# Optimization experiments

Measured on AMD Instinct MI355X. Metric: run time of the kernel, lower is better.

The kernel has to match this reference:

```python
import jax, jax.numpy as jnp
import numpy as np

H = 256
W = 256
RADIUS = 1.5
TAU = 1.0
EPS = 1e-8


def _ndc_grid(h, w):
    ys, xs = jnp.meshgrid(jnp.arange(h, dtype=jnp.float32), jnp.arange(w, dtype=jnp.float32), indexing='ij')
    xs = xs / (w - 1) * 2.0 - 1.0
    ys = ys / (h - 1) * 2.0 - 1.0
    return jnp.stack([xs.ravel(), ys.ravel()], 0)  # [2, N]


def _make_rt(key, b, v):
    # near-identity extrinsics: identity rotation + small random translation
    t = jax.random.normal(key, (b, v, 3), dtype=jnp.float32) * 0.05
    rt = jnp.tile(jnp.eye(4, dtype=jnp.float32), (b, v, 1, 1))
    rt = rt.at[:, :, :3, 3].set(t)
    return rt


def setup_inputs() -> dict:
    key = jax.random.key(0)
    ks = jax.random.split(key, 4)
    B, V, C = 2, 3, 32
    depths = jax.random.uniform(ks[0], (B, V, 1, H, W), jnp.float32, 1.0, 3.0)
    feats = jax.random.normal(ks[1], (B, V, C, H, W), jnp.float32)
    K = jnp.tile(jnp.eye(4, dtype=jnp.float32), (B, 1, 1))
    K = K.at[:, 0, 0].set(1.2).at[:, 1, 1].set(1.2)  # NDC-space focal lengths
    src_RTs = _make_rt(ks[2], B, V)
    src_RTinvs = jnp.linalg.inv(src_RTs)
    dst_RTs = _make_rt(ks[3], B, 1)
    dst_RTinvs = jnp.linalg.inv(dst_RTs)
    return {"depths": depths, "feats": feats, "K": K, "src_RTs": src_RTs,
            "src_RTinvs": src_RTinvs, "dst_RTs": dst_RTs, "dst_RTinvs": dst_RTinvs}


def _view_to_world(depth, K_inv, RTinv):
    # depth: [BV, 1, N] -> world homogeneous coords [BV, 4, N]
    grid = _ndc_grid(H, W)                                      # [2, N]
    xy = grid[None] * depth                                     # [BV, 2, N]
    pc = jnp.concatenate([xy, depth, jnp.ones_like(depth)], 1)  # [BV, 4, N]
    cam = jnp.einsum('bij,bjn->bin', K_inv, pc)
    return jnp.einsum('bij,bjn->bin', RTinv, cam)


def _world_to_view(wrld, K, RT):
    cam = jnp.einsum('bij,bjn->bin', RT, wrld)
    proj = jnp.einsum('bij,bjn->bin', K, cam)
    z = proj[:, 2:3]
    xy = proj[:, 0:2] / (z + EPS)
    xy = jnp.where(z <= 0.0, -10.0, xy)       # invalid points pushed off-screen
    return jnp.concatenate([xy, z], 1)        # [BV, 3, N]


def _splatter(pc, feats, radius):
    # pc: [BV, N, 3] (x_ndc, y_ndc, depth); feats: [BV, C, N]
    BV, N, _ = pc.shape
    C = feats.shape[1]
    x, y, z = pc[..., 0], pc[..., 1], pc[..., 2]
    px = (x + 1.0) * 0.5 * (W - 1)
    py = (y + 1.0) * 0.5 * (H - 1)
    offs = jnp.array([[dy, dx] for dy in (-1, 0, 1) for dx in (-1, 0, 1)], dtype=jnp.float32)
    ix = jnp.round(px)[..., None] + offs[:, 1]     # [BV, N, 9]
    iy = jnp.round(py)[..., None] + offs[:, 0]
    dist = jnp.sqrt((ix - px[..., None]) ** 2 + (iy - py[..., None]) ** 2 + EPS)
    w_r = jnp.maximum(0.0, 1.0 - dist / radius)    # radius-based falloff
    valid = (ix >= 0) & (ix < W) & (iy >= 0) & (iy < H) & (z[..., None] > 0)
    w_d = jnp.exp(-TAU * z)[..., None]             # depth-aware (soft z-buffer) weight
    w = w_r * w_d * valid.astype(w_r.dtype)        # [BV, N, 9]
    idx = iy.astype(jnp.int32).clip(0, H - 1) * W + ix.astype(jnp.int32).clip(0, W - 1)
    flat = (jnp.arange(BV, dtype=jnp.int32)[:, None, None] * (H * W) + idx).reshape(-1)
    w_sum = jax.ops.segment_sum(w.reshape(-1), flat, num_segments=BV * H * W)
    fw = (feats[:, :, :, None] * w[:, None, :, :]).transpose(0, 2, 3, 1).reshape(-1, C)
    f_sum = jax.ops.segment_sum(fw, flat, num_segments=BV * H * W)
    z_sum = jax.ops.segment_sum((z[..., None] * w).reshape(-1), flat, num_segments=BV * H * W)
    out_f = (f_sum / (w_sum[:, None] + EPS)).reshape(BV, H, W, C).transpose(0, 3, 1, 2)
    out_d = (z_sum / (w_sum + EPS)).reshape(BV, 1, H, W)
    return out_f, out_d


def reference(depths, feats, K, src_RTs, src_RTinvs, dst_RTs, dst_RTinvs):
    B, V, C = feats.shape[0], feats.shape[1], feats.shape[2]
    N = H * W
    d = depths.reshape(B * V, 1, N)
    f = feats.reshape(B * V, C, N)
    K_bv = jnp.repeat(K, V, axis=0)
    K_inv_bv = jnp.repeat(jnp.linalg.inv(K), V, axis=0)
    src_rtinv = src_RTinvs.reshape(B * V, 4, 4)
    dst_rt = jnp.repeat(dst_RTs[:, 0], V, axis=0)
    wrld = _view_to_world(d, K_inv_bv, src_rtinv)      # view -> world per source view
    sampler = _world_to_view(wrld, K_bv, dst_rt)       # world -> target view [BV,3,N]
    pc = sampler.transpose(0, 2, 1)                    # [BV, N, 3]
    prj_f, prj_d = _splatter(pc, f, RADIUS)
    return prj_f.reshape(B, V, C, H, W), prj_d.reshape(B, V, 1, H, W)
```

## Files before the change

### kernel.cpp

```cpp
#include <hip/hip_runtime.h>
#include <hip/hip_fp16.h>
#include <math.h>

#define H 256
#define W 256
#define HW (H * W)
#define B 2
#define V 3
#define BV (B * V)
#define C 32
#define RADIUS 1.5f
#define TAU 1.0f
#define EPS 1e-8f

#define NPIX (BV * HW)
#define NBLK (NPIX / 256)
#define CAP 16
#define OVF_CAP 65536

__device__ __forceinline__ int swizzle_block(int bid) {
    return (bid & 7) * (NBLK / 8) + (bid >> 3);
}

__global__ void setup_kernel(const float* __restrict__ Kmat,
                             const float* __restrict__ srcRTinv,
                             const float* __restrict__ dstRT,
                             float* __restrict__ Mbuf) {
    int bv = threadIdx.x;
    if (bv >= BV) return;
    int b = bv / V;

    float a[4][8];
    for (int i = 0; i < 4; i++)
        for (int j = 0; j < 4; j++) {
            a[i][j] = Kmat[b * 16 + i * 4 + j];
            a[i][4 + j] = (i == j) ? 1.0f : 0.0f;
        }
    for (int col = 0; col < 4; col++) {
        int piv = col;
        float best = fabsf(a[col][col]);
        for (int r = col + 1; r < 4; r++) {
            float v = fabsf(a[r][col]);
            if (v > best) { best = v; piv = r; }
        }
        if (piv != col) {
            for (int j = 0; j < 8; j++) {
                float t = a[col][j]; a[col][j] = a[piv][j]; a[piv][j] = t;
            }
        }
        float s = 1.0f / a[col][col];
        for (int j = 0; j < 8; j++) a[col][j] *= s;
        for (int r = 0; r < 4; r++) {
            if (r == col) continue;
            float m = a[r][col];
            for (int j = 0; j < 8; j++) a[r][j] -= m * a[col][j];
        }
    }
    float Kinv[16];
    for (int i = 0; i < 4; i++)
        for (int j = 0; j < 4; j++) Kinv[i * 4 + j] = a[i][4 + j];

    float T1[16];
    const float* S = srcRTinv + bv * 16;
    for (int i = 0; i < 4; i++)
        for (int j = 0; j < 4; j++) {
            float acc = 0.0f;
            for (int k = 0; k < 4; k++) acc += S[i * 4 + k] * Kinv[k * 4 + j];
            T1[i * 4 + j] = acc;
        }
    float T2[16];
    const float* D = dstRT + b * 16;
    for (int i = 0; i < 4; i++)
        for (int j = 0; j < 4; j++) {
            float acc = 0.0f;
            for (int k = 0; k < 4; k++) acc += D[i * 4 + k] * T1[k * 4 + j];
            T2[i * 4 + j] = acc;
        }
    const float* Kb = Kmat + b * 16;
    for (int i = 0; i < 4; i++)
        for (int j = 0; j < 4; j++) {
            float acc = 0.0f;
            for (int k = 0; k < 4; k++) acc += Kb[i * 4 + k] * T2[k * 4 + j];
            Mbuf[bv * 16 + i * 4 + j] = acc;
        }
}

template <typename F>
__device__ __forceinline__ void for_each_tap(float px, float py, float z, F&& fn) {
    if (!(z > 0.0f)) return;
    float rx = rintf(px), ry = rintf(py);
#pragma unroll
    for (int dy = -1; dy <= 1; dy++) {
#pragma unroll
        for (int dx = -1; dx <= 1; dx++) {
            float ix = rx + (float)dx, iy = ry + (float)dy;
            if (ix >= 0.0f && ix < (float)W && iy >= 0.0f && iy < (float)H) {
                float ddx = ix - px, ddy = iy - py;
                float d2 = ddx * ddx + ddy * ddy + EPS;
                if (d2 < RADIUS * RADIUS) {
                    int q = ((int)iy << 8) | (int)ix;
                    fn(q);
                }
            }
        }
    }
}

__global__ __launch_bounds__(256) void project_fill_kernel(
    const float* __restrict__ depths, const float* __restrict__ Mbuf,
    int* __restrict__ counts, unsigned short* __restrict__ bins16,
    int* __restrict__ ovf_cnt, int2* __restrict__ ovf) {
    int gid = swizzle_block(blockIdx.x) * 256 + threadIdx.x;
    int bv = gid >> 16;
    int n = gid & (HW - 1);
    int pxi = n & (W - 1);
    int pyi = n >> 8;

    float xn = (float)pxi * (2.0f / (W - 1)) - 1.0f;
    float yn = (float)pyi * (2.0f / (H - 1)) - 1.0f;
    float d = depths[gid];
    const float* M = Mbuf + bv * 16;
    float X = xn * d, Y = yn * d;
    float p0 = M[0] * X + M[1] * Y + M[2] * d + M[3];
    float p1 = M[4] * X + M[5] * Y + M[6] * d + M[7];
    float z  = M[8] * X + M[9] * Y + M[10] * d + M[11];

    bool zpos = z > 0.0f;
    float inv = 1.0f / (z + EPS);
    float xp = zpos ? p0 * inv : -10.0f;
    float yp = zpos ? p1 * inv : -10.0f;
    float px = (xp + 1.0f) * 0.5f * (float)(W - 1);
    float py = (yp + 1.0f) * 0.5f * (float)(H - 1);

    int base = bv << 16;
    for_each_tap(px, py, z, [&](int q) {
        int g = base | q;
        int slot = atomicAdd(&counts[g], 1);
        if (slot < CAP) {
            bins16[(size_t)g * CAP + slot] = (unsigned short)n;
        } else {
            int o = atomicAdd(ovf_cnt, 1);
            if (o < OVF_CAP) ovf[o] = make_int2(g, n);
        }
    });
}

__global__ __launch_bounds__(256) void transpose_kernel(
    const float* __restrict__ feats, __half* __restrict__ featsT) {
    __shared__ float sm[C][257];
    int blk = blockIdx.x;
    int bv = blk >> 8;
    int n0 = (blk & 255) << 8;
    int tid = threadIdx.x;
    const float* src = feats + (size_t)bv * C * HW + n0;
#pragma unroll
    for (int c = 0; c < C; c++) sm[c][tid] = src[(size_t)c * HW + tid];
    __syncthreads();
    __half* dst = featsT + ((size_t)bv * HW + n0) * C;
#pragma unroll
    for (int pass = 0; pass < 8; pass++) {
        int nl = pass * 32 + (tid >> 3);
        int c4 = (tid & 7) << 2;
        __half2 lo = __floats2half2_rn(sm[c4][nl], sm[c4 + 1][nl]);
        __half2 hi = __floats2half2_rn(sm[c4 + 2][nl], sm[c4 + 3][nl]);
        uint2 pk;
        pk.x = *(unsigned int*)&lo;
        pk.y = *(unsigned int*)&hi;
        *(uint2*)(dst + (size_t)nl * C + c4) = pk;
    }
}

__global__ __launch_bounds__(256) void gather_kernel(
    const float* __restrict__ depths, const float* __restrict__ Mbuf,
    const __half* __restrict__ featsT, const int* __restrict__ counts,
    const unsigned short* __restrict__ bins16,
    const int* __restrict__ ovf_cnt, const int2* __restrict__ ovf,
    float* __restrict__ out) {
    int gid = swizzle_block(blockIdx.x) * 256 + threadIdx.x;
    int bv = gid >> 16;
    int q = gid & (HW - 1);
    float qx = (float)(q & (W - 1));
    float qy = (float)(q >> 8);

    int cnt = counts[gid];
    int cap = min(cnt, CAP);

    const float* M = Mbuf + bv * 16;
    float m00 = M[0], m01 = M[1], m02 = M[2],  m03 = M[3];
    float m10 = M[4], m11 = M[5], m12 = M[6],  m13 = M[7];
    float m20 = M[8], m21 = M[9], m22 = M[10], m23 = M[11];

    const float* dep = depths + ((size_t)bv << 16);
    const __half* fb = featsT + ((size_t)bv << 16) * C;

    float wsum = 0.0f, zwsum = 0.0f;
    float facc[C];
#pragma unroll
    for (int c = 0; c < C; c++) facc[c] = 0.0f;

    auto accumulate = [&](int n) {
        float d = dep[n];
        float xn = (float)(n & (W - 1)) * (2.0f / (W - 1)) - 1.0f;
        float yn = (float)(n >> 8)      * (2.0f / (H - 1)) - 1.0f;
        float X = xn * d, Y = yn * d;
        float p0 = m00 * X + m01 * Y + m02 * d + m03;
        float p1 = m10 * X + m11 * Y + m12 * d + m13;
        float z  = m20 * X + m21 * Y + m22 * d + m23;
        float inv = 1.0f / (z + EPS);
        float px = (p0 * inv + 1.0f) * 0.5f * (float)(W - 1);
        float py = (p1 * inv + 1.0f) * 0.5f * (float)(H - 1);
        float ddx = qx - px, ddy = qy - py;
        float dist = sqrtf(ddx * ddx + ddy * ddy + EPS);
        float wr = fmaxf(0.0f, 1.0f - dist * (1.0f / RADIUS));
        float w = wr * expf(-TAU * z);
        wsum += w;
        zwsum += z * w;
        const uint4* fp = (const uint4*)(fb + (size_t)n * C);
#pragma unroll
        for (int g = 0; g < 4; g++) {
            uint4 v = fp[g];
            const __half2* h2 = (const __half2*)&v;
#pragma unroll
            for (int k = 0; k < 4; k++) {
                float2 f2 = __half22float2(h2[k]);
                facc[g * 8 + 2 * k]     = fmaf(w, f2.x, facc[g * 8 + 2 * k]);
                facc[g * 8 + 2 * k + 1] = fmaf(w, f2.y, facc[g * 8 + 2 * k + 1]);
            }
        }
    };

    const uint4* bp = (const uint4*)(bins16 + (size_t)gid * CAP);
    uint4 r0 = bp[0];
    uint4 r1 = bp[1];
    auto do2 = [&](unsigned int wv, int j0) {
        if (j0 < cap)     accumulate((int)(wv & 0xffffu));
        if (j0 + 1 < cap) accumulate((int)(wv >> 16));
    };
    do2(r0.x, 0);  do2(r0.y, 2);  do2(r0.z, 4);  do2(r0.w, 6);
    do2(r1.x, 8);  do2(r1.y, 10); do2(r1.z, 12); do2(r1.w, 14);

    if (cnt > CAP) {
        int oc = min(*ovf_cnt, OVF_CAP);
        for (int i = 0; i < oc; i++) {
            int2 e = ovf[i];
            if (e.x == gid) accumulate(e.y);
        }
    }

    float invw = 1.0f / (wsum + EPS);
    float* ob = out + (size_t)bv * C * HW + q;
#pragma unroll
    for (int c = 0; c < C; c++) ob[(size_t)c * HW] = facc[c] * invw;
    out[(size_t)BV * C * HW + gid] = zwsum * invw;
}

extern "C" void kernel_launch(void* const* d_in, const int* in_sizes, int n_in,
                              void* d_out, int out_size, void* d_ws, size_t ws_size,
                              hipStream_t stream) {
    const float* depths   = (const float*)d_in[0];
    const float* feats    = (const float*)d_in[1];
    const float* Kmat     = (const float*)d_in[2];
    const float* srcRTinv = (const float*)d_in[4];
    const float* dstRT    = (const float*)d_in[5];
    float* out = (float*)d_out;

    char* ws = (char*)d_ws;
    size_t off_bins = 0;
    size_t off_featsT = off_bins + (size_t)CAP * NPIX * 2;
    size_t off_counts = off_featsT + (size_t)NPIX * C * 2;
    size_t off_ovfcnt = off_counts + (size_t)NPIX * 4;
    size_t off_ovf = off_ovfcnt + 16;
    size_t off_M = off_ovf + (size_t)OVF_CAP * 8;
    size_t needed = off_M + (size_t)BV * 16 * 4;

    if (ws_size < needed) {
        hipMemsetAsync(d_out, 0, (size_t)out_size * 4, stream);
        return;
    }

    unsigned short* bins16 = (unsigned short*)(ws + off_bins);
    __half* featsT = (__half*)(ws + off_featsT);
    int* counts    = (int*)(ws + off_counts);
    int* ovf_cnt   = (int*)(ws + off_ovfcnt);
    int2* ovf      = (int2*)(ws + off_ovf);
    float* Mbuf    = (float*)(ws + off_M);

    hipMemsetAsync(counts, 0, (size_t)NPIX * 4 + 16, stream);
    setup_kernel<<<1, 64, 0, stream>>>(Kmat, srcRTinv, dstRT, Mbuf);
    project_fill_kernel<<<NBLK, 256, 0, stream>>>(depths, Mbuf, counts, bins16,
                                                  ovf_cnt, ovf);
    transpose_kernel<<<NBLK, 256, 0, stream>>>(feats, featsT);
    gather_kernel<<<NBLK, 256, 0, stream>>>(depths, Mbuf, featsT, counts,
                                            bins16, ovf_cnt, ovf, out);
}
```

Baseline: 210.0 us.

## Bin each projected point once by nearest cell; gather scans 3x3 neighborhood

The fill pass now does one atomic insert per source point into its nearest pixel cell, on a padded grid, instead of up to nine atomics into per-target bins. The cell entry stores the index together with the depth. The gather kernel scans the 3x3 neighbouring cells, recomputes the projection, and skips points whose radial weight is zero. This removes most scatter atomics and the separate depth reload. In exchange, gather now reads nine counters and more candidate entries per pixel, and the per-cell capacity is smaller, so more points may spill into the linearly scanned overflow list.

Measured after the change: 197.1 us. -6.2%, faster.

```diff
diff --git a/kernel.cpp b/kernel.cpp
--- a/kernel.cpp
+++ b/kernel.cpp
@@ -15,7 +15,11 @@
 
 #define NPIX (BV * HW)
 #define NBLK (NPIX / 256)
-#define CAP 16
+
+#define GW 258
+#define GH 258
+#define NCELL (BV * GH * GW)
+#define CCAP 8
 #define OVF_CAP 65536
 
 __device__ __forceinline__ int swizzle_block(int bid) {
@@ -85,31 +89,10 @@
         }
 }
 
-template <typename F>
-__device__ __forceinline__ void for_each_tap(float px, float py, float z, F&& fn) {
-    if (!(z > 0.0f)) return;
-    float rx = rintf(px), ry = rintf(py);
-#pragma unroll
-    for (int dy = -1; dy <= 1; dy++) {
-#pragma unroll
-        for (int dx = -1; dx <= 1; dx++) {
-            float ix = rx + (float)dx, iy = ry + (float)dy;
-            if (ix >= 0.0f && ix < (float)W && iy >= 0.0f && iy < (float)H) {
-                float ddx = ix - px, ddy = iy - py;
-                float d2 = ddx * ddx + ddy * ddy + EPS;
-                if (d2 < RADIUS * RADIUS) {
-                    int q = ((int)iy << 8) | (int)ix;
-                    fn(q);
-                }
-            }
-        }
-    }
-}
-
 __global__ __launch_bounds__(256) void project_fill_kernel(
     const float* __restrict__ depths, const float* __restrict__ Mbuf,
-    int* __restrict__ counts, unsigned short* __restrict__ bins16,
-    int* __restrict__ ovf_cnt, int2* __restrict__ ovf) {
+    int* __restrict__ counts, float2* __restrict__ cells,
+    int* __restrict__ ovf_cnt, int4* __restrict__ ovf) {
     int gid = swizzle_block(blockIdx.x) * 256 + threadIdx.x;
     int bv = gid >> 16;
     int n = gid & (HW - 1);
@@ -125,24 +108,24 @@
     float p1 = M[4] * X + M[5] * Y + M[6] * d + M[7];
     float z  = M[8] * X + M[9] * Y + M[10] * d + M[11];
 
-    bool zpos = z > 0.0f;
+    if (!(z > 0.0f)) return;
     float inv = 1.0f / (z + EPS);
-    float xp = zpos ? p0 * inv : -10.0f;
-    float yp = zpos ? p1 * inv : -10.0f;
-    float px = (xp + 1.0f) * 0.5f * (float)(W - 1);
-    float py = (yp + 1.0f) * 0.5f * (float)(H - 1);
-
-    int base = bv << 16;
-    for_each_tap(px, py, z, [&](int q) {
-        int g = base | q;
-        int slot = atomicAdd(&counts[g], 1);
-        if (slot < CAP) {
-            bins16[(size_t)g * CAP + slot] = (unsigned short)n;
-        } else {
-            int o = atomicAdd(ovf_cnt, 1);
-            if (o < OVF_CAP) ovf[o] = make_int2(g, n);
-        }
-    });
+    float px = (p0 * inv + 1.0f) * 0.5f * (float)(W - 1);
+    float py = (p1 * inv + 1.0f) * 0.5f * (float)(H - 1);
+    float rx = rintf(px), ry = rintf(py);
+    if (rx < -1.0f || rx > (float)W || ry < -1.0f || ry > (float)H) return;
+
+    int cell = bv * (GH * GW) + ((int)ry + 1) * GW + ((int)rx + 1);
+    int slot = atomicAdd(&counts[cell], 1);
+    if (slot < CCAP) {
+        float2 e;
+        e.x = __uint_as_float((unsigned int)n);
+        e.y = d;
+        cells[(size_t)cell * CCAP + slot] = e;
+    } else {
+        int o = atomicAdd(ovf_cnt, 1);
+        if (o < OVF_CAP) ovf[o] = make_int4(cell, n, __float_as_int(d), 0);
+    }
 }
 
 __global__ __launch_bounds__(256) void transpose_kernel(
@@ -171,10 +154,9 @@
 }
 
 __global__ __launch_bounds__(256) void gather_kernel(
-    const float* __restrict__ depths, const float* __restrict__ Mbuf,
-    const __half* __restrict__ featsT, const int* __restrict__ counts,
-    const unsigned short* __restrict__ bins16,
-    const int* __restrict__ ovf_cnt, const int2* __restrict__ ovf,
+    const float* __restrict__ Mbuf, const __half* __restrict__ featsT,
+    const int* __restrict__ counts, const float2* __restrict__ cells,
+    const int* __restrict__ ovf_cnt, const int4* __restrict__ ovf,
     float* __restrict__ out) {
     int gid = swizzle_block(blockIdx.x) * 256 + threadIdx.x;
     int bv = gid >> 16;
@@ -182,15 +164,11 @@
     float qx = (float)(q & (W - 1));
     float qy = (float)(q >> 8);
 
-    int cnt = counts[gid];
-    int cap = min(cnt, CAP);
-
     const float* M = Mbuf + bv * 16;
     float m00 = M[0], m01 = M[1], m02 = M[2],  m03 = M[3];
     float m10 = M[4], m11 = M[5], m12 = M[6],  m13 = M[7];
     float m20 = M[8], m21 = M[9], m22 = M[10], m23 = M[11];
 
-    const float* dep = depths + ((size_t)bv << 16);
     const __half* fb = featsT + ((size_t)bv << 16) * C;
 
     float wsum = 0.0f, zwsum = 0.0f;
@@ -198,8 +176,7 @@
 #pragma unroll
     for (int c = 0; c < C; c++) facc[c] = 0.0f;
 
-    auto accumulate = [&](int n) {
-        float d = dep[n];
+    auto accumulate = [&](int n, float d) {
         float xn = (float)(n & (W - 1)) * (2.0f / (W - 1)) - 1.0f;
         float yn = (float)(n >> 8)      * (2.0f / (H - 1)) - 1.0f;
         float X = xn * d, Y = yn * d;
@@ -212,38 +189,46 @@
         float ddx = qx - px, ddy = qy - py;
         float dist = sqrtf(ddx * ddx + ddy * ddy + EPS);
         float wr = fmaxf(0.0f, 1.0f - dist * (1.0f / RADIUS));
-        float w = wr * expf(-TAU * z);
-        wsum += w;
-        zwsum += z * w;
-        const uint4* fp = (const uint4*)(fb + (size_t)n * C);
-#pragma unroll
-        for (int g = 0; g < 4; g++) {
-            uint4 v = fp[g];
-            const __half2* h2 = (const __half2*)&v;
-#pragma unroll
-            for (int k = 0; k < 4; k++) {
-                float2 f2 = __half22float2(h2[k]);
-                facc[g * 8 + 2 * k]     = fmaf(w, f2.x, facc[g * 8 + 2 * k]);
-                facc[g * 8 + 2 * k + 1] = fmaf(w, f2.y, facc[g * 8 + 2 * k + 1]);
+        if (wr > 0.0f) {
+            float w = wr * expf(-TAU * z);
+            wsum += w;
+            zwsum += z * w;
+            const uint4* fp = (const uint4*)(fb + (size_t)n * C);
+#pragma unroll
+            for (int g = 0; g < 4; g++) {
+                uint4 v = fp[g];
+                const __half2* h2 = (const __half2*)&v;
+#pragma unroll
+                for (int k = 0; k < 4; k++) {
+                    float2 f2 = __half22float2(h2[k]);
+                    facc[g * 8 + 2 * k]     = fmaf(w, f2.x, facc[g * 8 + 2 * k]);
+                    facc[g * 8 + 2 * k + 1] = fmaf(w, f2.y, facc[g * 8 + 2 * k + 1]);
+                }
             }
         }
     };
 
-    const uint4* bp = (const uint4*)(bins16 + (size_t)gid * CAP);
-    uint4 r0 = bp[0];
-    uint4 r1 = bp[1];
-    auto do2 = [&](unsigned int wv, int j0) {
-        if (j0 < cap)     accumulate((int)(wv & 0xffffu));
-        if (j0 + 1 < cap) accumulate((int)(wv >> 16));
-    };
-    do2(r0.x, 0);  do2(r0.y, 2);  do2(r0.z, 4);  do2(r0.w, 6);
-    do2(r1.x, 8);  do2(r1.y, 10); do2(r1.z, 12); do2(r1.w, 14);
-
-    if (cnt > CAP) {
-        int oc = min(*ovf_cnt, OVF_CAP);
-        for (int i = 0; i < oc; i++) {
-            int2 e = ovf[i];
-            if (e.x == gid) accumulate(e.y);
+    int cbase = bv * (GH * GW);
+#pragma unroll
+    for (int dy = 0; dy < 3; dy++) {
+        int rowbase = cbase + (q / W + dy) * GW + (q & (W - 1));
+#pragma unroll
+        for (int dx = 0; dx < 3; dx++) {
+            int cell = rowbase + dx;
+            int cc = counts[cell];
+            int m = min(cc, CCAP);
+            const float2* e = cells + (size_t)cell * CCAP;
+            for (int j = 0; j < m; j++) {
+                float2 v = e[j];
+                accumulate((int)__float_as_uint(v.x), v.y);
+            }
+            if (cc > CCAP) {
+                int oc = min(*ovf_cnt, OVF_CAP);
+                for (int i = 0; i < oc; i++) {
+                    int4 t = ovf[i];
+                    if (t.x == cell) accumulate(t.y, __int_as_float(t.z));
+                }
+            }
         }
     }
 
@@ -265,12 +250,12 @@
     float* out = (float*)d_out;
 
     char* ws = (char*)d_ws;
-    size_t off_bins = 0;
-    size_t off_featsT = off_bins + (size_t)CAP * NPIX * 2;
+    size_t off_cells = 0;
+    size_t off_featsT = off_cells + (size_t)NCELL * CCAP * 8;
     size_t off_counts = off_featsT + (size_t)NPIX * C * 2;
-    size_t off_ovfcnt = off_counts + (size_t)NPIX * 4;
+    size_t off_ovfcnt = off_counts + (size_t)NCELL * 4;
     size_t off_ovf = off_ovfcnt + 16;
-    size_t off_M = off_ovf + (size_t)OVF_CAP * 8;
+    size_t off_M = off_ovf + (size_t)OVF_CAP * 16;
     size_t needed = off_M + (size_t)BV * 16 * 4;
 
     if (ws_size < needed) {
@@ -278,18 +263,18 @@
         return;
     }
 
-    unsigned short* bins16 = (unsigned short*)(ws + off_bins);
+    float2* cells  = (float2*)(ws + off_cells);
     __half* featsT = (__half*)(ws + off_featsT);
     int* counts    = (int*)(ws + off_counts);
     int* ovf_cnt   = (int*)(ws + off_ovfcnt);
-    int2* ovf      = (int2*)(ws + off_ovf);
+    int4* ovf      = (int4*)(ws + off_ovf);
     float* Mbuf    = (float*)(ws + off_M);
 
-    hipMemsetAsync(counts, 0, (size_t)NPIX * 4 + 16, stream);
+    hipMemsetAsync(counts, 0, (size_t)NCELL * 4 + 16, stream);
     setup_kernel<<<1, 64, 0, stream>>>(Kmat, srcRTinv, dstRT, Mbuf);
-    project_fill_kernel<<<NBLK, 256, 0, stream>>>(depths, Mbuf, counts, bins16,
+    project_fill_kernel<<<NBLK, 256, 0, stream>>>(depths, Mbuf, counts, cells,
                                                   ovf_cnt, ovf);
     transpose_kernel<<<NBLK, 256, 0, stream>>>(feats, featsT);
-    gather_kernel<<<NBLK, 256, 0, stream>>>(depths, Mbuf, featsT, counts,
-                                            bins16, ovf_cnt, ovf, out);
-}
+    gather_kernel<<<NBLK, 256, 0, stream>>>(Mbuf, featsT, counts, cells,
+                                            ovf_cnt, ovf, out);
+}
```
